# Kernel optimization log

Measured on AMD Instinct MI355X. Metric: run time of the kernel, lower is better.

## Reference

```python
import jax, jax.numpy as jnp
import numpy as np

NUM_GRAPHS = 128
NODES_PER_GRAPH = 512
NUM_NODES = NUM_GRAPHS * NODES_PER_GRAPH
NUM_EDGES = NUM_NODES * 16
IN_DIM = 64
HID = 128
NUM_HEADS = 4
BN_EPS = 1e-5


def setup_inputs() -> dict:
    key = jax.random.key(0)
    ks = jax.random.split(key, 12)
    x = jax.random.normal(ks[0], (NUM_NODES, IN_DIM), dtype=jnp.float32)
    edge_index = jax.random.randint(ks[1], (2, NUM_EDGES), 0, NUM_NODES, dtype=jnp.int32)
    batch = jnp.repeat(jnp.arange(NUM_GRAPHS, dtype=jnp.int32), NODES_PER_GRAPH)
    s = 0.05
    W0 = jax.random.normal(ks[2], (IN_DIM, HID), dtype=jnp.float32) * s
    b0 = jnp.zeros((HID,), jnp.float32)
    Wh = jax.random.normal(ks[3], (3, HID, HID), dtype=jnp.float32) * s  # convs 1..3
    bh = jnp.zeros((3, HID), jnp.float32)
    bn_gamma = jnp.ones((4, HID), jnp.float32)
    bn_beta = jnp.zeros((4, HID), jnp.float32)
    bn_mean = jnp.zeros((4, HID), jnp.float32)
    bn_var = jnp.ones((4, HID), jnp.float32)
    attn_in_w = jax.random.normal(ks[4], (3 * HID, HID), dtype=jnp.float32) * s
    attn_in_b = jnp.zeros((3 * HID,), jnp.float32)
    attn_out_w = jax.random.normal(ks[5], (HID, HID), dtype=jnp.float32) * s
    attn_out_b = jnp.zeros((HID,), jnp.float32)
    return dict(x=x, W0=W0, b0=b0, Wh=Wh, bh=bh, bn_gamma=bn_gamma, bn_beta=bn_beta,
                bn_mean=bn_mean, bn_var=bn_var, attn_in_w=attn_in_w, attn_in_b=attn_in_b,
                attn_out_w=attn_out_w, attn_out_b=attn_out_b, edge_index=edge_index, batch=batch)


def _forward(x, W0, b0, Wh, bh, bn_gamma, bn_beta, bn_mean, bn_var,
             attn_in_w, attn_in_b, attn_out_w, attn_out_b, edge_index, batch):
    N = x.shape[0]
    src, dst = edge_index[0], edge_index[1]
    # GCN symmetric normalization with self-loops (PyG GCNConv)
    deg = jax.ops.segment_sum(jnp.ones_like(src, jnp.float32), dst, num_segments=N) + 1.0
    dis = jax.lax.rsqrt(deg)                      # deg^{-1/2}
    enorm = (dis[src] * dis[dst])[:, None]        # per-edge norm
    self_norm = (dis * dis)[:, None]              # self-loop norm

    def gcn(h, W, b):
        h = h @ W
        agg = jax.ops.segment_sum(h[src] * enorm, dst, num_segments=N)
        return agg + h * self_norm + b

    def bn(h, i):
        scale = bn_gamma[i] * jax.lax.rsqrt(bn_var[i] + BN_EPS)
        return (h - bn_mean[i]) * scale + bn_beta[i]  # eval-mode BN

    # dropout is identity in eval mode
    h = jax.nn.relu(bn(gcn(x, W0, b0), 0))
    h = jax.nn.relu(bn(gcn(h, Wh[0], bh[0]), 1))
    h = jax.nn.relu(bn(gcn(h, Wh[1], bh[1]), 2))
    f = jax.nn.relu(bn(gcn(h, Wh[2], bh[2]), 3))   # [N, HID]

    # per-graph self-attention (equal-size contiguous graphs -> batched MHA)
    dh = HID // NUM_HEADS
    xg = f.reshape(NUM_GRAPHS, NODES_PER_GRAPH, HID)
    qkv = xg @ attn_in_w.T + attn_in_b            # [G, n, 3H]
    q, k, v = jnp.split(qkv, 3, axis=-1)

    def heads(t):
        return t.reshape(NUM_GRAPHS, NODES_PER_GRAPH, NUM_HEADS, dh).transpose(0, 2, 1, 3)
    q, k, v = heads(q), heads(k), heads(v)
    scores = jnp.einsum('ghnd,ghmd->ghnm', q, k) / np.sqrt(dh).astype(np.float32)
    attn = jax.nn.softmax(scores, axis=-1)
    o = jnp.einsum('ghnm,ghmd->ghnd', attn, v).transpose(0, 2, 1, 3).reshape(NUM_GRAPHS, NODES_PER_GRAPH, HID)
    o = o @ attn_out_w.T + attn_out_b
    final = o.reshape(N, HID)

    # global mean pool over batch indices
    cnt = jax.ops.segment_sum(jnp.ones((N,), jnp.float32), batch, num_segments=NUM_GRAPHS)
    graph_emb = jax.ops.segment_sum(final, batch, num_segments=NUM_GRAPHS) / cnt[:, None]
    return final, graph_emb


def reference(x, W0, b0, Wh, bh, bn_gamma, bn_beta, bn_mean, bn_var,
              attn_in_w, attn_in_b, attn_out_w, attn_out_b, edge_index, batch):
    return _forward(x, W0, b0, Wh, bh, bn_gamma, bn_beta, bn_mean, bn_var,
                    attn_in_w, attn_in_b, attn_out_w, attn_out_b, edge_index, batch)
```

## Files before the change

### kernel.cpp

```cpp
#include <hip/hip_runtime.h>
#include <hip/hip_bf16.h>
#include <cstdint>
#include <cstddef>

#define N_NODES 65536
#define N_EDGES 1048576
#define N_GRAPHS 128
#define NPG 512
#define IN_DIM 64
#define HID 128
#define BN_EPS 1e-5f

typedef __attribute__((ext_vector_type(8))) short bf16x8;
typedef __attribute__((ext_vector_type(4))) float f32x4;
typedef __attribute__((ext_vector_type(8))) unsigned short u16x8;
typedef __attribute__((ext_vector_type(4))) unsigned int u32x4;

__device__ inline unsigned short f2bf(float f) {
  unsigned u = __builtin_bit_cast(unsigned, f);
  u = u + 0x7fffu + ((u >> 16) & 1u);
  return (unsigned short)(u >> 16);
}
__device__ inline float bf2f(unsigned short h) {
  unsigned u = ((unsigned)h) << 16;
  return __builtin_bit_cast(float, u);
}
__device__ inline void split_bf(float v, unsigned short& hi, unsigned short& lo) {
  hi = f2bf(v);
  lo = f2bf(v - bf2f(hi));
}
__device__ inline void split_bf_fast(float v, unsigned short& hi, unsigned short& lo) {
  unsigned u = __builtin_bit_cast(unsigned, v);
  hi = (unsigned short)(u >> 16);
  float r = v - __builtin_bit_cast(float, u & 0xffff0000u);
  lo = f2bf(r);
}
__device__ inline unsigned cvt_pk_bf16(float a, float b) {
  unsigned r;
  asm("v_cvt_pk_bf16_f32 %0, %1, %2" : "=v"(r) : "v"(a), "v"(b));
  return r;
}
__device__ inline void split2_pk(float a, float b, unsigned& hpk, unsigned& lpk) {
  hpk = cvt_pk_bf16(a, b);
  float ha = __builtin_bit_cast(float, hpk << 16);
  float hb = __builtin_bit_cast(float, hpk & 0xffff0000u);
  lpk = cvt_pk_bf16(a - ha, b - hb);
}

__global__ __launch_bounds__(256) void hist_kernel(const int* __restrict__ dst,
                                                   int* __restrict__ deg) {
  int e = blockIdx.x * 256 + threadIdx.x;
  if (e < N_EDGES) atomicAdd(&deg[dst[e]], 1);
}

__global__ __launch_bounds__(256) void dis_kernel(const int* __restrict__ deg,
                                                  float* __restrict__ dis) {
  int n = blockIdx.x * 256 + threadIdx.x;
  if (n < N_NODES) dis[n] = 1.0f / sqrtf((float)deg[n] + 1.0f);
}

__global__ __launch_bounds__(1024) void scan_kernel(const int* __restrict__ deg,
                                                    int* __restrict__ offsets,
                                                    int* __restrict__ cursor) {
  __shared__ int sums[1024];
  int t = threadIdx.x;
  int base = t * 64;
  const int4* dp = (const int4*)(deg + base);
  int s = 0;
#pragma unroll
  for (int i = 0; i < 16; i++) {
    int4 v = dp[i];
    s += v.x + v.y + v.z + v.w;
  }
  sums[t] = s;
  __syncthreads();
  for (int off = 1; off < 1024; off <<= 1) {
    int v = (t >= off) ? sums[t - off] : 0;
    __syncthreads();
    sums[t] += v;
    __syncthreads();
  }
  int run = (t == 0) ? 0 : sums[t - 1];
#pragma unroll
  for (int i = 0; i < 16; i++) {
    int4 v = dp[i];
    int idx = base + i * 4;
    offsets[idx] = run; cursor[idx] = run; run += v.x;
    offsets[idx + 1] = run; cursor[idx + 1] = run; run += v.y;
    offsets[idx + 2] = run; cursor[idx + 2] = run; run += v.z;
    offsets[idx + 3] = run; cursor[idx + 3] = run; run += v.w;
  }
  if (t == 1023) offsets[N_NODES] = run;
}

__global__ __launch_bounds__(256) void fill_kernel(const int* __restrict__ src,
                                                   const int* __restrict__ dst,
                                                   int* __restrict__ cursor,
                                                   int* __restrict__ csr) {
  int e = blockIdx.x * 256 + threadIdx.x;
  if (e < N_EDGES) {
    int d = dst[e];
    int slot = atomicAdd(&cursor[d], 1);
    csr[slot] = src[e];
  }
}

__global__ __launch_bounds__(256) void agg64_kernel(const float* __restrict__ x,
                                                    const float* __restrict__ dis,
                                                    const int* __restrict__ offsets,
                                                    const int* __restrict__ csr,
                                                    unsigned short* __restrict__ zhi,
                                                    unsigned short* __restrict__ zlo) {
  int node = blockIdx.x * 4 + (threadIdx.x >> 6);
  int lane = threadIdx.x & 63;
  float dn = dis[node];
  float acc = x[(size_t)node * 64 + lane] * dn * dn;
  int beg = offsets[node], end = offsets[node + 1];
  int k = beg;
  for (; k + 8 <= end; k += 8) {
    int s[8];
#pragma unroll
    for (int i = 0; i < 8; i++) s[i] = csr[k + i];
    float w[8];
#pragma unroll
    for (int i = 0; i < 8; i++) w[i] = dn * dis[s[i]];
    float v[8];
#pragma unroll
    for (int i = 0; i < 8; i++) v[i] = x[(size_t)s[i] * 64 + lane];
#pragma unroll
    for (int i = 0; i < 8; i++) acc = fmaf(w[i], v[i], acc);
  }
  for (; k < end; k++) {
    int s = csr[k];
    acc = fmaf(dn * dis[s], x[(size_t)s * 64 + lane], acc);
  }
  unsigned short h_, l_;
  split_bf(acc, h_, l_);
  zhi[(size_t)node * 64 + lane] = h_;
  zlo[(size_t)node * 64 + lane] = l_;
}

__global__ __launch_bounds__(256) void agg128_kernel(const float* __restrict__ h,
                                                     const float* __restrict__ dis,
                                                     const int* __restrict__ offsets,
                                                     const int* __restrict__ csr,
                                                     unsigned short* __restrict__ zhi,
                                                     unsigned short* __restrict__ zlo) {
  int node = blockIdx.x * 4 + (threadIdx.x >> 6);
  int lane = threadIdx.x & 63;
  float dn = dis[node];
  float sn = dn * dn;
  const float* hr = h + (size_t)node * 128;
  float a0 = hr[lane] * sn;
  float a1 = hr[lane + 64] * sn;
  int beg = offsets[node], end = offsets[node + 1];
  int k = beg;
  for (; k + 8 <= end; k += 8) {
    int s[8];
#pragma unroll
    for (int i = 0; i < 8; i++) s[i] = csr[k + i];
    float w[8];
#pragma unroll
    for (int i = 0; i < 8; i++) w[i] = dn * dis[s[i]];
    float u[8], d[8];
#pragma unroll
    for (int i = 0; i < 8; i++) {
      const float* p = h + (size_t)s[i] * 128;
      u[i] = p[lane];
      d[i] = p[lane + 64];
    }
#pragma unroll
    for (int i = 0; i < 8; i++) {
      a0 = fmaf(w[i], u[i], a0);
      a1 = fmaf(w[i], d[i], a1);
    }
  }
  for (; k < end; k++) {
    int s = csr[k];
    float w = dn * dis[s];
    const float* hs = h + (size_t)s * 128;
    a0 = fmaf(w, hs[lane], a0);
    a1 = fmaf(w, hs[lane + 64], a1);
  }
  unsigned short h0, l0, h1, l1;
  split_bf(a0, h0, l0);
  split_bf(a1, h1, l1);
  zhi[(size_t)node * 128 + lane] = h0;
  zlo[(size_t)node * 128 + lane] = l0;
  zhi[(size_t)node * 128 + lane + 64] = h1;
  zlo[(size_t)node * 128 + lane + 64] = l1;
}

template <bool TRANS>
__global__ __launch_bounds__(256) void wprep_kernel(const float* __restrict__ W, int K, int O,
                                                    unsigned short* __restrict__ hi,
                                                    unsigned short* __restrict__ lo) {
  int idx = blockIdx.x * 256 + threadIdx.x;
  int KC = K / 32;
  int total = (O / 16) * KC * 64;
  if (idx >= total) return;
  int lane = idx & 63;
  int rest = idx >> 6;
  int kc = rest % KC;
  int nt = rest / KC;
  int n = nt * 16 + (lane & 15);
  int kb = kc * 32 + (lane >> 4) * 8;
  unsigned short* hp = hi + (size_t)idx * 8;
  unsigned short* lp = lo + (size_t)idx * 8;
#pragma unroll
  for (int j = 0; j < 8; j++) {
    int k = kb + j;
    float v = TRANS ? W[(size_t)n * K + k] : W[(size_t)k * O + n];
    unsigned short h_, l_;
    split_bf(v, h_, l_);
    hp[j] = h_;
    lp[j] = l_;
  }
}

template <int K, int O, bool DOBN, bool DORELU, bool SPLIT_OUT, bool GROUPED,
          bool DOPOOL = false>
__global__ __launch_bounds__(256) void gemm_mfma(
    const unsigned short* __restrict__ Ahi, const unsigned short* __restrict__ Alo,
    const unsigned short* __restrict__ Whi, const unsigned short* __restrict__ Wlo,
    const float* __restrict__ bias,
    const float* __restrict__ gamma, const float* __restrict__ beta,
    const float* __restrict__ mean, const float* __restrict__ var,
    float* __restrict__ Cf, unsigned short* __restrict__ Chi,
    unsigned short* __restrict__ Clo, float* __restrict__ Pool = nullptr) {
  constexpr int KC = K / 32;
  int wave = threadIdx.x >> 6;
  int lane = threadIdx.x & 63;
  int m0 = blockIdx.x * 128 + wave * 32;
  int o0 = blockIdx.y * 128;
  int mrow = lane & 15;
  int kseg = (lane >> 4) * 8;

  f32x4 acc[2][8];
#pragma unroll
  for (int mt = 0; mt < 2; mt++)
#pragma unroll
    for (int nt = 0; nt < 8; nt++) acc[mt][nt] = (f32x4)0.0f;

#pragma unroll
  for (int kc = 0; kc < KC; kc++) {
    bf16x8 ah[2], al[2];
#pragma unroll
    for (int mt = 0; mt < 2; mt++) {
      size_t aoff = (size_t)(m0 + mt * 16 + mrow) * K + kc * 32 + kseg;
      ah[mt] = *(const bf16x8*)(Ahi + aoff);
      al[mt] = *(const bf16x8*)(Alo + aoff);
    }
#pragma unroll
    for (int nt = 0; nt < 8; nt++) {
      size_t foff = (((size_t)(blockIdx.y * 8 + nt) * KC + kc) * 64 + lane) * 8;
      bf16x8 bh = *(const bf16x8*)(Whi + foff);
      bf16x8 bl = *(const bf16x8*)(Wlo + foff);
#pragma unroll
      for (int mt = 0; mt < 2; mt++) {
        acc[mt][nt] = __builtin_amdgcn_mfma_f32_16x16x32_bf16(ah[mt], bh, acc[mt][nt], 0, 0, 0);
        acc[mt][nt] = __builtin_amdgcn_mfma_f32_16x16x32_bf16(ah[mt], bl, acc[mt][nt], 0, 0, 0);
        acc[mt][nt] = __builtin_amdgcn_mfma_f32_16x16x32_bf16(al[mt], bh, acc[mt][nt], 0, 0, 0);
        acc[mt][nt] = __builtin_amdgcn_mfma_f32_16x16x32_bf16(al[mt], bl, acc[mt][nt], 0, 0, 0);
      }
    }
  }

  int ccol = lane & 15;
  int crow0 = (lane >> 4) * 4;
  float colsum[8];
  if constexpr (DOPOOL) {
#pragma unroll
    for (int nt = 0; nt < 8; nt++) colsum[nt] = 0.0f;
  }
#pragma unroll
  for (int nt = 0; nt < 8; nt++) {
    int c = o0 + nt * 16 + ccol;
    float sc, cb;
    float b = bias[c];
    if (DOBN) {
      sc = gamma[c] * rsqrtf(var[c] + BN_EPS);
      cb = (b - mean[c]) * sc + beta[c];
    } else {
      sc = 1.0f;
      cb = b;
    }
#pragma unroll
    for (int mt = 0; mt < 2; mt++) {
#pragma unroll
      for (int r = 0; r < 4; r++) {
        float v = fmaf(acc[mt][nt][r], sc, cb);
        if (DORELU) v = fmaxf(v, 0.0f);
        size_t row = (size_t)(m0 + mt * 16 + crow0 + r);
        if (SPLIT_OUT) {
          unsigned short h_, l_;
          split_bf(v, h_, l_);
          if (GROUPED) {
            size_t base = row * (size_t)(2 * O) + (size_t)(((c >> 5) << 6) + (c & 31));
            Chi[base] = h_;
            Chi[base + 32] = l_;
          } else {
            Chi[row * O + c] = h_;
            Clo[row * O + c] = l_;
          }
        } else {
          Cf[row * O + c] = v;
        }
        if constexpr (DOPOOL) colsum[nt] += v;
      }
    }
  }
  if constexpr (DOPOOL) {
    __shared__ float pb[4][128];
#pragma unroll
    for (int nt = 0; nt < 8; nt++) {
      float cs = colsum[nt];
      cs += __shfl_xor(cs, 16, 64);
      cs += __shfl_xor(cs, 32, 64);
      if ((lane >> 4) == 0) pb[wave][nt * 16 + ccol] = cs;
    }
    __syncthreads();
    int tt = threadIdx.x;
    if (tt < 128) {
      float s2 = pb[0][tt] + pb[1][tt] + pb[2][tt] + pb[3][tt];
      int gg = blockIdx.x >> 2;
      atomicAdd(&Pool[gg * 128 + tt], s2 * (1.0f / NPG));
    }
  }
}

__global__ __launch_bounds__(256) void knorm_kernel(const unsigned short* __restrict__ qvs,
                                                    float* __restrict__ kmax2) {
  int g = blockIdx.x >> 2;
  int h = blockIdx.x & 3;
  size_t gbase = (size_t)g * NPG;
  float best = 0.0f;
#pragma unroll
  for (int r = 0; r < 2; r++) {
    int j = r * 256 + threadIdx.x;
    size_t base = (gbase + j) * 768 + (size_t)(4 + h) * 64;
    float s = 0.0f;
#pragma unroll
    for (int i = 0; i < 4; i++) {
      u16x8 hh = *(const u16x8*)(qvs + base + i * 8);
      u16x8 ll = *(const u16x8*)(qvs + base + 32 + i * 8);
#pragma unroll
      for (int jj = 0; jj < 8; jj++) {
        float v = bf2f(hh[jj]) + bf2f(ll[jj]);
        s = fmaf(v, v, s);
      }
    }
    best = fmaxf(best, s);
  }
#pragma unroll
  for (int off = 32; off >= 1; off >>= 1)
    best = fmaxf(best, __shfl_xor(best, off, 64));
  __shared__ float red[4];
  int wave = threadIdx.x >> 6;
  if ((threadIdx.x & 63) == 0) red[wave] = best;
  __syncthreads();
  if (threadIdx.x == 0) {
    float m = fmaxf(fmaxf(red[0], red[1]), fmaxf(red[2], red[3]));
    kmax2[blockIdx.x] = m;
  }
}

__global__ __launch_bounds__(256, 2) void attn_mfma_kernel(
    const unsigned short* __restrict__ qvs, const float* __restrict__ kmax2,
    unsigned short* __restrict__ ohi, unsigned short* __restrict__ olo) {
  int wb = ((blockIdx.x & 7) << 7) | (blockIdx.x >> 3);
  int g = wb >> 3;
  int h = (wb >> 1) & 3;
  int half = wb & 1;
  int t = threadIdx.x;
  int wave = t >> 6;
  int lane = t & 63;
  int quad = lane >> 4;
  int l15 = lane & 15;
  size_t gbase = (size_t)g * NPG;
  int qb = half * 256 + wave * 64;

  const float cf = 0.17677669529663687f * 1.4426950408889634f;

  __shared__ unsigned short Kh[2][32][40] __attribute__((aligned(16)));
  __shared__ unsigned short Kl[2][32][40] __attribute__((aligned(16)));
  __shared__ unsigned short Vh[2][33][40] __attribute__((aligned(16)));
  __shared__ unsigned short Vl[2][33][40] __attribute__((aligned(16)));
  __shared__ float Ot[64 * 36] __attribute__((aligned(16)));

  bf16x8 qh[4], ql[4];
  float Mq[4];
  float km2 = kmax2[g * 4 + h];
#pragma unroll
  for (int mt = 0; mt < 4; mt++) {
    size_t qoff = (gbase + qb + mt * 16 + l15) * 768 + (size_t)h * 64 + quad * 8;
    u16x8 hh = *(const u16x8*)(qvs + qoff);
    u16x8 ll = *(const u16x8*)(qvs + qoff + 32);
    qh[mt] = __builtin_bit_cast(bf16x8, hh);
    ql[mt] = __builtin_bit_cast(bf16x8, ll);
    float s = 0.0f;
#pragma unroll
    for (int j = 0; j < 8; j++) {
      float v = bf2f(hh[j]) + bf2f(ll[j]);
      s = fmaf(v, v, s);
    }
    s += __shfl_xor(s, 16);
    s += __shfl_xor(s, 32);
    Mq[mt] = cf * sqrtf(s * km2);
  }

  f32x4 Oa[4][3];
#pragma unroll
  for (int mt = 0; mt < 4; mt++)
#pragma unroll
    for (int nt = 0; nt < 3; nt++) Oa[mt][nt] = (f32x4)0.0f;

  if (t >= 64 && t < 72) {
    int u = t - 64;
    int bsel = u >> 2;
    int i = u & 3;
    u16x8 ones;
#pragma unroll
    for (int j = 0; j < 8; j++) ones[j] = 0x3F80;
    *(u16x8*)&Vh[bsel][32][i * 8] = ones;
  }

  bool isK = (t >= 128);
  bool isV = (t < 64);
  u16x8 kreg_h, kreg_l;
  ushort4 vreg_h[4], vreg_l[4];
  int kkey = 0, vkeyb = 0, vdvb = 0;
  const unsigned short* kptr = nullptr;
  const unsigned short* vptr = nullptr;
  const size_t CSTRIDE = (size_t)32 * 768;
  if (isK) {
    int t2 = t - 128;
    kkey = t2 >> 2;
    int kds = (t2 & 3) * 8;
    int nt_ = kkey >> 4, q_ = (kkey >> 2) & 3, r_ = kkey & 3;
    int p_ = (nt_ << 1) | (r_ >> 1);
    int kphys = 8 * (q_ ^ p_) + 2 * p_ + (r_ & 1);
    kptr = qvs + (gbase + (size_t)kphys) * 768 + (size_t)(4 + h) * 64 + kds;
  } else if (isV) {
    vkeyb = (t & 7) * 4;
    vdvb = (t >> 3) * 4;
    vptr = qvs + (gbase + (size_t)vkeyb) * 768 + (size_t)(8 + h) * 64 + vdvb;
  }

  auto load_chunk = [&]() {
    if (isK) {
      kreg_h = *(const u16x8*)kptr;
      kreg_l = *(const u16x8*)(kptr + 32);
      kptr += CSTRIDE;
    } else if (isV) {
#pragma unroll
      for (int r = 0; r < 4; r++) {
        vreg_h[r] = *(const ushort4*)(vptr + (size_t)r * 768);
        vreg_l[r] = *(const ushort4*)(vptr + (size_t)r * 768 + 32);
      }
      vptr += CSTRIDE;
    }
  };

  auto stage_chunk = [&](int bsel) {
    if (isK) {
      int kds = ((t - 128) & 3) * 8;
      *(u16x8*)&Kh[bsel][kkey][kds] = kreg_h;
      *(u16x8*)&Kl[bsel][kkey][kds] = kreg_l;
    } else if (isV) {
      unsigned short ha[4][4], la[4][4];
#pragma unroll
      for (int r = 0; r < 4; r++) {
        *(ushort4*)&ha[r][0] = vreg_h[r];
        *(ushort4*)&la[r][0] = vreg_l[r];
      }
#pragma unroll
      for (int c2 = 0; c2 < 4; c2++) {
        ushort4 hv, lv;
        hv.x = ha[0][c2]; hv.y = ha[1][c2]; hv.z = ha[2][c2]; hv.w = ha[3][c2];
        lv.x = la[0][c2]; lv.y = la[1][c2]; lv.z = la[2][c2]; lv.w = la[3][c2];
        *(ushort4*)&Vh[bsel][vdvb + c2][vkeyb] = hv;
        *(ushort4*)&Vl[bsel][vdvb + c2][vkeyb] = lv;
      }
    }
  };

  load_chunk();
  stage_chunk(0);
  __syncthreads();

  int p = 0;
  for (int c = 0; c < 16; c++) {
    if (c < 15) load_chunk();

    bf16x8 akh[2], akl[2];
    akh[0] = *(const bf16x8*)&Kh[p][l15][quad * 8];
    akh[1] = *(const bf16x8*)&Kh[p][16 + l15][quad * 8];
    akl[0] = *(const bf16x8*)&Kl[p][l15][quad * 8];
    akl[1] = *(const bf16x8*)&Kl[p][16 + l15][quad * 8];
    bf16x8 bvh0 = *(const bf16x8*)&Vh[p][l15][quad * 8];
    bf16x8 bvl0 = *(const bf16x8*)&Vl[p][l15][quad * 8];
    bf16x8 bvh1 = *(const bf16x8*)&Vh[p][16 + l15][quad * 8];
    bf16x8 bvl1 = *(const bf16x8*)&Vl[p][16 + l15][quad * 8];
    bf16x8 bvh2 = *(const bf16x8*)&Vh[p][32 + l15][quad * 8];

#pragma unroll
    for (int mt = 0; mt < 4; mt++) {
      unsigned pkh[4], pkl[4];
#pragma unroll
      for (int nt = 0; nt < 2; nt++) {
        f32x4 S = (f32x4)0.0f;
        S = __builtin_amdgcn_mfma_f32_16x16x32_bf16(akh[nt], qh[mt], S, 0, 0, 0);
        S = __builtin_amdgcn_mfma_f32_16x16x32_bf16(akh[nt], ql[mt], S, 0, 0, 0);
        S = __builtin_amdgcn_mfma_f32_16x16x32_bf16(akl[nt], qh[mt], S, 0, 0, 0);
        S = __builtin_amdgcn_mfma_f32_16x16x32_bf16(akl[nt], ql[mt], S, 0, 0, 0);
        float p0 = __builtin_exp2f(fmaf(S[0], cf, -Mq[mt]));
        float p1 = __builtin_exp2f(fmaf(S[1], cf, -Mq[mt]));
        float p2 = __builtin_exp2f(fmaf(S[2], cf, -Mq[mt]));
        float p3 = __builtin_exp2f(fmaf(S[3], cf, -Mq[mt]));
        split2_pk(p0, p1, pkh[nt * 2], pkl[nt * 2]);
        split2_pk(p2, p3, pkh[nt * 2 + 1], pkl[nt * 2 + 1]);
      }
      u32x4 uh, ul;
      uh[0] = pkh[0];
      uh[1] = (unsigned)__shfl_xor((int)pkh[1], 16, 64);
      uh[2] = (unsigned)__shfl_xor((int)pkh[2], 32, 64);
      uh[3] = (unsigned)__shfl_xor((int)pkh[3], 48, 64);
      ul[0] = pkl[0];
      ul[1] = (unsigned)__shfl_xor((int)pkl[1], 16, 64);
      ul[2] = (unsigned)__shfl_xor((int)pkl[2], 32, 64);
      ul[3] = (unsigned)__shfl_xor((int)pkl[3], 48, 64);
      bf16x8 pa_h = __builtin_bit_cast(bf16x8, uh);
      bf16x8 pa_l = __builtin_bit_cast(bf16x8, ul);

      Oa[mt][0] = __builtin_amdgcn_mfma_f32_16x16x32_bf16(pa_h, bvh0, Oa[mt][0], 0, 0, 0);
      Oa[mt][0] = __builtin_amdgcn_mfma_f32_16x16x32_bf16(pa_h, bvl0, Oa[mt][0], 0, 0, 0);
      Oa[mt][0] = __builtin_amdgcn_mfma_f32_16x16x32_bf16(pa_l, bvh0, Oa[mt][0], 0, 0, 0);
      Oa[mt][1] = __builtin_amdgcn_mfma_f32_16x16x32_bf16(pa_h, bvh1, Oa[mt][1], 0, 0, 0);
      Oa[mt][1] = __builtin_amdgcn_mfma_f32_16x16x32_bf16(pa_h, bvl1, Oa[mt][1], 0, 0, 0);
      Oa[mt][1] = __builtin_amdgcn_mfma_f32_16x16x32_bf16(pa_l, bvh1, Oa[mt][1], 0, 0, 0);
      Oa[mt][2] = __builtin_amdgcn_mfma_f32_16x16x32_bf16(pa_h, bvh2, Oa[mt][2], 0, 0, 0);
      Oa[mt][2] = __builtin_amdgcn_mfma_f32_16x16x32_bf16(pa_l, bvh2, Oa[mt][2], 0, 0, 0);
    }

    if (c < 15) stage_chunk(p ^ 1);
    __syncthreads();
    p ^= 1;
  }

  for (int w = 0; w < 4; w++) {
    if (wave == w) {
#pragma unroll
      for (int mt = 0; mt < 4; mt++) {
#pragma unroll
        for (int r = 0; r < 4; r++) {
          int row = mt * 16 + quad * 4 + r;
          Ot[row * 36 + l15] = Oa[mt][0][r];
          Ot[row * 36 + 16 + l15] = Oa[mt][1][r];
          if (l15 == 0) Ot[row * 36 + 32] = Oa[mt][2][r];
        }
      }
      int row = lane;
      float inv = 1.0f / Ot[row * 36 + 32];
      size_t node = gbase + qb + row;
#pragma unroll
      for (int seg = 0; seg < 4; seg++) {
        float v0 = Ot[row * 36 + seg * 8 + 0] * inv;
        float v1 = Ot[row * 36 + seg * 8 + 1] * inv;
        float v2 = Ot[row * 36 + seg * 8 + 2] * inv;
        float v3 = Ot[row * 36 + seg * 8 + 3] * inv;
        float v4 = Ot[row * 36 + seg * 8 + 4] * inv;
        float v5 = Ot[row * 36 + seg * 8 + 5] * inv;
        float v6 = Ot[row * 36 + seg * 8 + 6] * inv;
        float v7 = Ot[row * 36 + seg * 8 + 7] * inv;
        unsigned h0, l0, h1, l1, h2, l2, h3, l3;
        split2_pk(v0, v1, h0, l0);
        split2_pk(v2, v3, h1, l1);
        split2_pk(v4, v5, h2, l2);
        split2_pk(v6, v7, h3, l3);
        u32x4 hw, lw;
        hw[0] = h0; hw[1] = h1; hw[2] = h2; hw[3] = h3;
        lw[0] = l0; lw[1] = l1; lw[2] = l2; lw[3] = l3;
        *(u32x4*)(ohi + node * 128 + h * 32 + seg * 8) = hw;
        *(u32x4*)(olo + node * 128 + h * 32 + seg * 8) = lw;
      }
    }
    __syncthreads();
  }
}

extern "C" void kernel_launch(void* const* d_in, const int* in_sizes, int n_in,
                              void* d_out, int out_size, void* d_ws, size_t ws_size,
                              hipStream_t stream) {
  (void)in_sizes; (void)n_in; (void)out_size; (void)ws_size;
  const float* x          = (const float*)d_in[0];
  const float* W0         = (const float*)d_in[1];
  const float* b0         = (const float*)d_in[2];
  const float* Wh         = (const float*)d_in[3];
  const float* bh         = (const float*)d_in[4];
  const float* bn_gamma   = (const float*)d_in[5];
  const float* bn_beta    = (const float*)d_in[6];
  const float* bn_mean    = (const float*)d_in[7];
  const float* bn_var     = (const float*)d_in[8];
  const float* attn_in_w  = (const float*)d_in[9];
  const float* attn_in_b  = (const float*)d_in[10];
  const float* attn_out_w = (const float*)d_in[11];
  const float* attn_out_b = (const float*)d_in[12];
  const int* edge_index   = (const int*)d_in[13];
  const int* src = edge_index;
  const int* dst = edge_index + N_EDGES;

  char* ws = (char*)d_ws;
  size_t off = 0;
  auto alloc = [&](size_t bytes) -> void* {
    void* p = ws + off;
    off += (bytes + 255) & ~(size_t)255;
    return p;
  };
  int*   deg     = (int*)alloc((size_t)N_NODES * 4);
  int*   offsets = (int*)alloc((size_t)(N_NODES + 1) * 4);
  int*   cursor  = (int*)alloc((size_t)N_NODES * 4);
  int*   csr     = (int*)alloc((size_t)N_EDGES * 4);
  float* dis     = (float*)alloc((size_t)N_NODES * 4);
  float* bufA    = (float*)alloc((size_t)N_NODES * HID * 4);
  unsigned short* zhi = (unsigned short*)alloc((size_t)N_NODES * HID * 2);
  unsigned short* zlo = (unsigned short*)alloc((size_t)N_NODES * HID * 2);
  unsigned short* qvs = (unsigned short*)alloc((size_t)N_NODES * 768 * 2);
  float* kmax2   = (float*)alloc((size_t)N_GRAPHS * 4 * 4);
  unsigned short* w0h = (unsigned short*)alloc(8192 * 2);
  unsigned short* w0l = (unsigned short*)alloc(8192 * 2);
  unsigned short* whh[3], *whl[3];
  for (int i = 0; i < 3; i++) {
    whh[i] = (unsigned short*)alloc(16384 * 2);
    whl[i] = (unsigned short*)alloc(16384 * 2);
  }
  unsigned short* wqh = (unsigned short*)alloc(49152 * 2);
  unsigned short* wql = (unsigned short*)alloc(49152 * 2);
  unsigned short* woh = (unsigned short*)alloc(16384 * 2);
  unsigned short* wol = (unsigned short*)alloc(16384 * 2);

  unsigned short* fhi = (unsigned short*)bufA;
  unsigned short* flo = fhi + (size_t)N_NODES * HID;

  float* fin = (float*)d_out;
  float* emb = fin + (size_t)N_NODES * HID;

  hipMemsetAsync(deg, 0, (size_t)N_NODES * 4, stream);
  hipMemsetAsync(emb, 0, (size_t)N_GRAPHS * HID * 4, stream);
  hist_kernel<<<N_EDGES / 256, 256, 0, stream>>>(dst, deg);
  dis_kernel<<<N_NODES / 256, 256, 0, stream>>>(deg, dis);
  scan_kernel<<<1, 1024, 0, stream>>>(deg, offsets, cursor);
  fill_kernel<<<N_EDGES / 256, 256, 0, stream>>>(src, dst, cursor, csr);

  wprep_kernel<false><<<4, 256, 0, stream>>>(W0, 64, 128, w0h, w0l);
  for (int i = 0; i < 3; i++)
    wprep_kernel<false><<<8, 256, 0, stream>>>(Wh + (size_t)i * HID * HID, 128, 128,
                                               whh[i], whl[i]);
  wprep_kernel<true><<<24, 256, 0, stream>>>(attn_in_w, 128, 384, wqh, wql);
  wprep_kernel<true><<<8, 256, 0, stream>>>(attn_out_w, 128, 128, woh, wol);

  dim3 ggrid(N_NODES / 128, 1);
  agg64_kernel<<<N_NODES / 4, 256, 0, stream>>>(x, dis, offsets, csr, zhi, zlo);
  gemm_mfma<64, 128, true, true, false, false><<<ggrid, 256, 0, stream>>>(
      zhi, zlo, w0h, w0l, b0, bn_gamma, bn_beta, bn_mean, bn_var, bufA, nullptr, nullptr);
  for (int L = 0; L < 2; L++) {
    agg128_kernel<<<N_NODES / 4, 256, 0, stream>>>(bufA, dis, offsets, csr, zhi, zlo);
    gemm_mfma<128, 128, true, true, false, false><<<ggrid, 256, 0, stream>>>(
        zhi, zlo, whh[L], whl[L], bh + (size_t)L * HID,
        bn_gamma + (size_t)(L + 1) * HID, bn_beta + (size_t)(L + 1) * HID,
        bn_mean + (size_t)(L + 1) * HID, bn_var + (size_t)(L + 1) * HID,
        bufA, nullptr, nullptr);
  }
  agg128_kernel<<<N_NODES / 4, 256, 0, stream>>>(bufA, dis, offsets, csr, zhi, zlo);
  gemm_mfma<128, 128, true, true, true, false><<<ggrid, 256, 0, stream>>>(
      zhi, zlo, whh[2], whl[2], bh + (size_t)2 * HID,
      bn_gamma + (size_t)3 * HID, bn_beta + (size_t)3 * HID,
      bn_mean + (size_t)3 * HID, bn_var + (size_t)3 * HID,
      nullptr, fhi, flo);
  dim3 qgrid(N_NODES / 128, 3);
  gemm_mfma<128, 384, false, false, true, true><<<qgrid, 256, 0, stream>>>(
      fhi, flo, wqh, wql, attn_in_b, nullptr, nullptr, nullptr, nullptr,
      nullptr, qvs, nullptr);
  knorm_kernel<<<N_GRAPHS * 4, 256, 0, stream>>>(qvs, kmax2);
  attn_mfma_kernel<<<N_GRAPHS * 4 * 2, 256, 0, stream>>>(qvs, kmax2, zhi, zlo);
  gemm_mfma<128, 128, false, false, false, false, true><<<ggrid, 256, 0, stream>>>(
      zhi, zlo, woh, wol, attn_out_b, nullptr, nullptr, nullptr, nullptr,
      fin, nullptr, nullptr, emb);
}
```

Measured before the change: 807.9 us.

## Fuse key-norm max into QKV GEMM and merge prep kernels

Computes the per-graph, per-head maximum key squared norm in the QKV GEMM epilogue from fp32 accumulators and combines it with an atomicMax, replacing the separate knorm kernel that re-read K from memory. Also folds the degree-normalisation computation into the scan kernel and merges six weight-prep launches into a single kernel. The aim is fewer launches and one less pass over the QKV buffer, at the cost of extra shuffles and atomics in the GEMM epilogue and slightly different key norms, since they now come from unsplit fp32 values.

```diff
diff --git a/kernel.cpp b/kernel.cpp
--- a/kernel.cpp
+++ b/kernel.cpp
@@ -29,12 +29,6 @@
   hi = f2bf(v);
   lo = f2bf(v - bf2f(hi));
 }
-__device__ inline void split_bf_fast(float v, unsigned short& hi, unsigned short& lo) {
-  unsigned u = __builtin_bit_cast(unsigned, v);
-  hi = (unsigned short)(u >> 16);
-  float r = v - __builtin_bit_cast(float, u & 0xffff0000u);
-  lo = f2bf(r);
-}
 __device__ inline unsigned cvt_pk_bf16(float a, float b) {
   unsigned r;
   asm("v_cvt_pk_bf16_f32 %0, %1, %2" : "=v"(r) : "v"(a), "v"(b));
@@ -53,15 +47,10 @@
   if (e < N_EDGES) atomicAdd(&deg[dst[e]], 1);
 }
 
-__global__ __launch_bounds__(256) void dis_kernel(const int* __restrict__ deg,
-                                                  float* __restrict__ dis) {
-  int n = blockIdx.x * 256 + threadIdx.x;
-  if (n < N_NODES) dis[n] = 1.0f / sqrtf((float)deg[n] + 1.0f);
-}
-
 __global__ __launch_bounds__(1024) void scan_kernel(const int* __restrict__ deg,
                                                     int* __restrict__ offsets,
-                                                    int* __restrict__ cursor) {
+                                                    int* __restrict__ cursor,
+                                                    float* __restrict__ dis) {
   __shared__ int sums[1024];
   int t = threadIdx.x;
   int base = t * 64;
@@ -89,6 +78,10 @@
     offsets[idx + 1] = run; cursor[idx + 1] = run; run += v.y;
     offsets[idx + 2] = run; cursor[idx + 2] = run; run += v.z;
     offsets[idx + 3] = run; cursor[idx + 3] = run; run += v.w;
+    dis[idx]     = 1.0f / sqrtf((float)v.x + 1.0f);
+    dis[idx + 1] = 1.0f / sqrtf((float)v.y + 1.0f);
+    dis[idx + 2] = 1.0f / sqrtf((float)v.z + 1.0f);
+    dis[idx + 3] = 1.0f / sqrtf((float)v.w + 1.0f);
   }
   if (t == 1023) offsets[N_NODES] = run;
 }
@@ -191,14 +184,10 @@
   zlo[(size_t)node * 128 + lane + 64] = l1;
 }
 
-template <bool TRANS>
-__global__ __launch_bounds__(256) void wprep_kernel(const float* __restrict__ W, int K, int O,
-                                                    unsigned short* __restrict__ hi,
-                                                    unsigned short* __restrict__ lo) {
-  int idx = blockIdx.x * 256 + threadIdx.x;
+__device__ inline void wprep_one(int idx, const float* __restrict__ W, int K, int O,
+                                 bool trans, unsigned short* __restrict__ hi,
+                                 unsigned short* __restrict__ lo) {
   int KC = K / 32;
-  int total = (O / 16) * KC * 64;
-  if (idx >= total) return;
   int lane = idx & 63;
   int rest = idx >> 6;
   int kc = rest % KC;
@@ -210,7 +199,7 @@
 #pragma unroll
   for (int j = 0; j < 8; j++) {
     int k = kb + j;
-    float v = TRANS ? W[(size_t)n * K + k] : W[(size_t)k * O + n];
+    float v = trans ? W[(size_t)n * K + k] : W[(size_t)k * O + n];
     unsigned short h_, l_;
     split_bf(v, h_, l_);
     hp[j] = h_;
@@ -218,8 +207,33 @@
   }
 }
 
+__global__ __launch_bounds__(256) void wprep_all(
+    const float* __restrict__ W0, const float* __restrict__ Wh,
+    const float* __restrict__ Wq, const float* __restrict__ Wo,
+    unsigned short* w0h, unsigned short* w0l,
+    unsigned short* whh0, unsigned short* whl0,
+    unsigned short* whh1, unsigned short* whl1,
+    unsigned short* whh2, unsigned short* whl2,
+    unsigned short* wqh, unsigned short* wql,
+    unsigned short* woh, unsigned short* wol) {
+  int b = blockIdx.x, t = threadIdx.x;
+  if (b < 4) {
+    wprep_one(b * 256 + t, W0, 64, 128, false, w0h, w0l);
+  } else if (b < 28) {
+    int i = (b - 4) >> 3;
+    int idx = ((b - 4) & 7) * 256 + t;
+    unsigned short* hh = (i == 0) ? whh0 : ((i == 1) ? whh1 : whh2);
+    unsigned short* ll = (i == 0) ? whl0 : ((i == 1) ? whl1 : whl2);
+    wprep_one(idx, Wh + (size_t)i * HID * HID, 128, 128, false, hh, ll);
+  } else if (b < 52) {
+    wprep_one((b - 28) * 256 + t, Wq, 128, 384, true, wqh, wql);
+  } else {
+    wprep_one((b - 52) * 256 + t, Wo, 128, 128, true, woh, wol);
+  }
+}
+
 template <int K, int O, bool DOBN, bool DORELU, bool SPLIT_OUT, bool GROUPED,
-          bool DOPOOL = false>
+          bool DOPOOL = false, bool DOKNORM = false>
 __global__ __launch_bounds__(256) void gemm_mfma(
     const unsigned short* __restrict__ Ahi, const unsigned short* __restrict__ Alo,
     const unsigned short* __restrict__ Whi, const unsigned short* __restrict__ Wlo,
@@ -227,7 +241,8 @@
     const float* __restrict__ gamma, const float* __restrict__ beta,
     const float* __restrict__ mean, const float* __restrict__ var,
     float* __restrict__ Cf, unsigned short* __restrict__ Chi,
-    unsigned short* __restrict__ Clo, float* __restrict__ Pool = nullptr) {
+    unsigned short* __restrict__ Clo, float* __restrict__ Pool = nullptr,
+    float* __restrict__ Kmax = nullptr) {
   constexpr int KC = K / 32;
   int wave = threadIdx.x >> 6;
   int lane = threadIdx.x & 63;
@@ -327,41 +342,38 @@
       atomicAdd(&Pool[gg * 128 + tt], s2 * (1.0f / NPG));
     }
   }
-}
-
-__global__ __launch_bounds__(256) void knorm_kernel(const unsigned short* __restrict__ qvs,
-                                                    float* __restrict__ kmax2) {
-  int g = blockIdx.x >> 2;
-  int h = blockIdx.x & 3;
-  size_t gbase = (size_t)g * NPG;
-  float best = 0.0f;
-#pragma unroll
-  for (int r = 0; r < 2; r++) {
-    int j = r * 256 + threadIdx.x;
-    size_t base = (gbase + j) * 768 + (size_t)(4 + h) * 64;
-    float s = 0.0f;
-#pragma unroll
-    for (int i = 0; i < 4; i++) {
-      u16x8 hh = *(const u16x8*)(qvs + base + i * 8);
-      u16x8 ll = *(const u16x8*)(qvs + base + 32 + i * 8);
-#pragma unroll
-      for (int jj = 0; jj < 8; jj++) {
-        float v = bf2f(hh[jj]) + bf2f(ll[jj]);
-        s = fmaf(v, v, s);
-      }
-    }
-    best = fmaxf(best, s);
-  }
-#pragma unroll
-  for (int off = 32; off >= 1; off >>= 1)
-    best = fmaxf(best, __shfl_xor(best, off, 64));
-  __shared__ float red[4];
-  int wave = threadIdx.x >> 6;
-  if ((threadIdx.x & 63) == 0) red[wave] = best;
-  __syncthreads();
-  if (threadIdx.x == 0) {
-    float m = fmaxf(fmaxf(red[0], red[1]), fmaxf(red[2], red[3]));
-    kmax2[blockIdx.x] = m;
+  if constexpr (DOKNORM) {
+    if (blockIdx.y == 1) {
+      float bb[8];
+#pragma unroll
+      for (int nt = 0; nt < 8; nt++) bb[nt] = bias[o0 + nt * 16 + ccol];
+      float hmax[4] = {0.0f, 0.0f, 0.0f, 0.0f};
+#pragma unroll
+      for (int mt = 0; mt < 2; mt++) {
+#pragma unroll
+        for (int r = 0; r < 4; r++) {
+#pragma unroll
+          for (int hh2 = 0; hh2 < 4; hh2++) {
+            float v0 = acc[mt][2 * hh2][r] + bb[2 * hh2];
+            float v1 = acc[mt][2 * hh2 + 1][r] + bb[2 * hh2 + 1];
+            float s = fmaf(v0, v0, v1 * v1);
+            s += __shfl_xor(s, 1);
+            s += __shfl_xor(s, 2);
+            s += __shfl_xor(s, 4);
+            s += __shfl_xor(s, 8);
+            hmax[hh2] = fmaxf(hmax[hh2], s);
+          }
+        }
+      }
+#pragma unroll
+      for (int hh2 = 0; hh2 < 4; hh2++) {
+        float m = hmax[hh2];
+        m = fmaxf(m, __shfl_xor(m, 16));
+        m = fmaxf(m, __shfl_xor(m, 32));
+        if (lane == 0)
+          atomicMax((int*)&Kmax[(blockIdx.x >> 2) * 4 + hh2], __float_as_int(m));
+      }
+    }
   }
 }
 
@@ -647,17 +659,14 @@
 
   hipMemsetAsync(deg, 0, (size_t)N_NODES * 4, stream);
   hipMemsetAsync(emb, 0, (size_t)N_GRAPHS * HID * 4, stream);
+  hipMemsetAsync(kmax2, 0, (size_t)N_GRAPHS * 4 * 4, stream);
+
+  wprep_all<<<60, 256, 0, stream>>>(W0, Wh, attn_in_w, attn_out_w,
+                                    w0h, w0l, whh[0], whl[0], whh[1], whl[1],
+                                    whh[2], whl[2], wqh, wql, woh, wol);
   hist_kernel<<<N_EDGES / 256, 256, 0, stream>>>(dst, deg);
-  dis_kernel<<<N_NODES / 256, 256, 0, stream>>>(deg, dis);
-  scan_kernel<<<1, 1024, 0, stream>>>(deg, offsets, cursor);
+  scan_kernel<<<1, 1024, 0, stream>>>(deg, offsets, cursor, dis);
   fill_kernel<<<N_EDGES / 256, 256, 0, stream>>>(src, dst, cursor, csr);
-
-  wprep_kernel<false><<<4, 256, 0, stream>>>(W0, 64, 128, w0h, w0l);
-  for (int i = 0; i < 3; i++)
-    wprep_kernel<false><<<8, 256, 0, stream>>>(Wh + (size_t)i * HID * HID, 128, 128,
-                                               whh[i], whl[i]);
-  wprep_kernel<true><<<24, 256, 0, stream>>>(attn_in_w, 128, 384, wqh, wql);
-  wprep_kernel<true><<<8, 256, 0, stream>>>(attn_out_w, 128, 128, woh, wol);
 
   dim3 ggrid(N_NODES / 128, 1);
   agg64_kernel<<<N_NODES / 4, 256, 0, stream>>>(x, dis, offsets, csr, zhi, zlo);
@@ -678,10 +687,9 @@
       bn_mean + (size_t)3 * HID, bn_var + (size_t)3 * HID,
       nullptr, fhi, flo);
   dim3 qgrid(N_NODES / 128, 3);
-  gemm_mfma<128, 384, false, false, true, true><<<qgrid, 256, 0, stream>>>(
+  gemm_mfma<128, 384, false, false, true, true, false, true><<<qgrid, 256, 0, stream>>>(
       fhi, flo, wqh, wql, attn_in_b, nullptr, nullptr, nullptr, nullptr,
-      nullptr, qvs, nullptr);
-  knorm_kernel<<<N_GRAPHS * 4, 256, 0, stream>>>(qvs, kmax2);
+      nullptr, qvs, nullptr, nullptr, kmax2);
   attn_mfma_kernel<<<N_GRAPHS * 4 * 2, 256, 0, stream>>>(qvs, kmax2, zhi, zlo);
   gemm_mfma<128, 128, false, false, false, false, true><<<ggrid, 256, 0, stream>>>(
       zhi, zlo, woh, wol, attn_out_b, nullptr, nullptr, nullptr, nullptr,
```

New measurement: 827.7 us. +2.4%, slower.
